# Optimization experiments

Measured on AMD Instinct MI355X. Metric: run time of the kernel, lower is better.

Reference implementation:

```python
import jax, jax.numpy as jnp
import numpy as np


def setup_inputs() -> dict:
    key = jax.random.key(0)
    k1, k2 = jax.random.split(key)
    _input = jax.random.normal(k1, (64, 8, 256, 256), dtype=jnp.float32)
    _filter = jax.random.normal(k2, (8, 8, 3, 3), dtype=jnp.float32)
    return {"_input": _input, "_filter": _filter}


def reference(_input, _filter):
    # The original module builds an im2col buffer with Python loops and does a
    # single GEMM; the math is exactly a stride-1, VALID-padding cross-correlation:
    #   out[n,m,i,j] = sum_{c,r,s} input[n,c,i+r,j+s] * filter[m,c,r,s]
    # Expressed as the efficient implicit-GEMM convolution primitive.
    out = jax.lax.conv_general_dilated(
        _input, _filter,
        window_strides=(1, 1),
        padding="VALID",
        dimension_numbers=("NCHW", "OIHW", "NCHW"),
    )
    return out  # (N, M, H-R+1, W-S+1)
```

## Files before the change

### kernel.cpp

```cpp
#include <hip/hip_runtime.h>


#define SLOT_HALFS (4 * 256 * 8)

typedef _Float16 half8 __attribute__((ext_vector_type(8)));
typedef float floatx4 __attribute__((ext_vector_type(4)));

__global__ __launch_bounds__(256, 3)
void conv2d_mfma_kernel(const float* __restrict__ inp,
                        const float* __restrict__ filt,
                        float* __restrict__ out) {
    __shared__ __align__(16) _Float16 s_in[3 * SLOT_HALFS + 64];

    const int tid    = threadIdx.x;
    const int ystrip = blockIdx.x * 32;
    const int n      = blockIdx.y;

    const float* in_n  = inp + (size_t)n * (8 * 256 * 256);
    float*       out_n = out + (size_t)n * (8 * 254 * 254);

    const int lane = tid & 63;
    const int w    = tid >> 6;
    const int lx   = lane & 15;
    const int g    = lane >> 4;

    half8 afrag[3];
    int roff[3], soff[3];
    #pragma unroll
    for (int kk = 0; kk < 3; ++kk) {
        int q  = kk * 4 + g;
        int qa = q > 8 ? 8 : q;
        roff[kk] = qa / 3;
        soff[kk] = qa - roff[kk] * 3;
        half8 a = {};
        if (q <= 8 && lx < 8) {
            #pragma unroll
            for (int j = 0; j < 8; ++j)
                a[j] = (_Float16)filt[lx * 72 + j * 9 + q];
        }
        afrag[kk] = a;
    }

    float v[4][8];
    auto load_chunk = [&](int ck) {
        #pragma unroll
        for (int k = 0; k < 4; ++k) {
            const int  iy = ystrip + ck * 4 + k;
            const bool ok = iy < 256;
            const float* p = in_n + iy * 256 + tid;
            #pragma unroll
            for (int c = 0; c < 8; ++c)
                v[k][c] = ok ? p[c * 65536] : 0.0f;
        }
    };
    auto write_chunk = [&](int ck) {
        _Float16* base = &s_in[(ck % 3) * SLOT_HALFS];
        #pragma unroll
        for (int k = 0; k < 4; ++k) {
            half8 h;
            #pragma unroll
            for (int c = 0; c < 8; ++c) h[c] = (_Float16)v[k][c];
            *reinterpret_cast<half8*>(&base[(k * 256 + tid) * 8]) = h;
        }
    };

    load_chunk(0); write_chunk(0);
    load_chunk(1); write_chunk(1);
    __syncthreads();

    for (int t = 0; t < 8; ++t) {
        if (t < 7) load_chunk(t + 2);

        const int ro = t * 4 + w;
        const int oy = ystrip + ro;

        const _Float16* bptr[3];
        #pragma unroll
        for (int kk = 0; kk < 3; ++kk) {
            int L    = ro + roff[kk];
            int slot = (L >> 2) % 3;
            bptr[kk] = &s_in[slot * SLOT_HALFS +
                             ((L & 3) * 256 + lx + soff[kk]) * 8];
        }

        const bool do_store = (g < 2) && (oy < 254);
        #pragma unroll
        for (int xg = 0; xg < 16; ++xg) {
            floatx4 acc = {0.0f, 0.0f, 0.0f, 0.0f};
            #pragma unroll
            for (int kk = 0; kk < 3; ++kk) {
                const half8 b =
                    *reinterpret_cast<const half8*>(bptr[kk] + xg * 128);
                acc = __builtin_amdgcn_mfma_f32_16x16x32_f16(
                          afrag[kk], b, acc, 0, 0, 0);
            }
            const int ox = xg * 16 + lx;
            if (do_store && ox < 254) {
                float* op = out_n + (g * 4) * 64516 + oy * 254 + ox;
                #pragma unroll
                for (int i = 0; i < 4; ++i)
                    op[i * 64516] = acc[i];
            }
        }

        if (t < 7) write_chunk(t + 2);
        __syncthreads();
    }
}

extern "C" void kernel_launch(void* const* d_in, const int* in_sizes, int n_in,
                              void* d_out, int out_size, void* d_ws, size_t ws_size,
                              hipStream_t stream) {
    const float* inp  = (const float*)d_in[0];
    const float* filt = (const float*)d_in[1];
    float* outp = (float*)d_out;

    dim3 grid(8, 64, 1);
    dim3 block(256);
    conv2d_mfma_kernel<<<grid, block, 0, stream>>>(inp, filt, outp);
}
```

Measured before the change: 306.8 us.

## Vectorize global loads, swizzle LDS layout, and stage output through shared memory

```diff
diff --git a/kernel.cpp b/kernel.cpp
--- a/kernel.cpp
+++ b/kernel.cpp
@@ -1,16 +1,17 @@
 #include <hip/hip_runtime.h>
 
-
-#define SLOT_HALFS (4 * 256 * 8)
 
 typedef _Float16 half8 __attribute__((ext_vector_type(8)));
 typedef float floatx4 __attribute__((ext_vector_type(4)));
 
-__global__ __launch_bounds__(256, 3)
+#define SLOT_H 8192
+
+__global__ __launch_bounds__(256, 2)
 void conv2d_mfma_kernel(const float* __restrict__ inp,
                         const float* __restrict__ filt,
                         float* __restrict__ out) {
-    __shared__ __align__(16) _Float16 s_in[3 * SLOT_HALFS + 64];
+    __shared__ __align__(16) _Float16 s_in[3 * SLOT_H];
+    __shared__ __align__(16) float    s_out[4 * 2048];
 
     const int tid    = threadIdx.x;
     const int ystrip = blockIdx.x * 32;
@@ -23,15 +24,24 @@
     const int w    = tid >> 6;
     const int lx   = lane & 15;
     const int g    = lane >> 4;
+    const int lx4  = tid & 63;
 
     half8 afrag[3];
-    int roff[3], soff[3];
+    int   roff[3];
+    int   loH[3][4];
     #pragma unroll
     for (int kk = 0; kk < 3; ++kk) {
         int q  = kk * 4 + g;
         int qa = q > 8 ? 8 : q;
         roff[kk] = qa / 3;
-        soff[kk] = qa - roff[kk] * 3;
+        int soff = qa - roff[kk] * 3;
+        int q0   = lx + soff;
+        int e    = (q0 & 3) ^ ((q0 >> 2) & 3);
+        int q0b  = q0 >> 4;
+        int baseH = (q0 >> 2) * 32;
+        #pragma unroll
+        for (int j = 0; j < 4; ++j)
+            loH[kk][j] = baseH + ((e ^ ((j + q0b) & 3)) << 3);
         half8 a = {};
         if (q <= 8 && lx < 8) {
             #pragma unroll
@@ -41,26 +51,28 @@
         afrag[kk] = a;
     }
 
-    float v[4][8];
+    float4 vv[8];
     auto load_chunk = [&](int ck) {
-        #pragma unroll
-        for (int k = 0; k < 4; ++k) {
-            const int  iy = ystrip + ck * 4 + k;
-            const bool ok = iy < 256;
-            const float* p = in_n + iy * 256 + tid;
+        const int iy = ystrip + ck * 4 + w;
+        if (iy < 256) {
+            const float* p = in_n + iy * 256 + lx4 * 4;
             #pragma unroll
             for (int c = 0; c < 8; ++c)
-                v[k][c] = ok ? p[c * 65536] : 0.0f;
+                vv[c] = *reinterpret_cast<const float4*>(p + c * 65536);
+        } else {
+            #pragma unroll
+            for (int c = 0; c < 8; ++c) vv[c] = make_float4(0.f,0.f,0.f,0.f);
         }
     };
     auto write_chunk = [&](int ck) {
-        _Float16* base = &s_in[(ck % 3) * SLOT_HALFS];
+        _Float16* base = &s_in[(ck % 3) * SLOT_H + w * 2048 + lx4 * 32];
+        const int sw = (lx4 & 3) ^ ((lx4 >> 2) & 3);
         #pragma unroll
-        for (int k = 0; k < 4; ++k) {
+        for (int i = 0; i < 4; ++i) {
             half8 h;
             #pragma unroll
-            for (int c = 0; c < 8; ++c) h[c] = (_Float16)v[k][c];
-            *reinterpret_cast<half8*>(&base[(k * 256 + tid) * 8]) = h;
+            for (int c = 0; c < 8; ++c) h[c] = (_Float16)vv[c][i];
+            *reinterpret_cast<half8*>(base + ((i ^ sw) << 3)) = h;
         }
     };
 
@@ -70,36 +82,47 @@
 
     for (int t = 0; t < 8; ++t) {
         if (t < 7) load_chunk(t + 2);
+        __builtin_amdgcn_sched_barrier(0);
 
         const int ro = t * 4 + w;
         const int oy = ystrip + ro;
 
-        const _Float16* bptr[3];
+        int ab[3][4];
         #pragma unroll
         for (int kk = 0; kk < 3; ++kk) {
             int L    = ro + roff[kk];
-            int slot = (L >> 2) % 3;
-            bptr[kk] = &s_in[slot * SLOT_HALFS +
-                             ((L & 3) * 256 + lx + soff[kk]) * 8];
+            int rbH  = ((L >> 2) % 3) * SLOT_H + (L & 3) * 2048;
+            #pragma unroll
+            for (int j = 0; j < 4; ++j) ab[kk][j] = rbH + loH[kk][j];
         }
 
-        const bool do_store = (g < 2) && (oy < 254);
+        const bool do_out = (g < 2) && (oy < 254);
         #pragma unroll
         for (int xg = 0; xg < 16; ++xg) {
-            floatx4 acc = {0.0f, 0.0f, 0.0f, 0.0f};
+            floatx4 acc = {0.f, 0.f, 0.f, 0.f};
             #pragma unroll
             for (int kk = 0; kk < 3; ++kk) {
-                const half8 b =
-                    *reinterpret_cast<const half8*>(bptr[kk] + xg * 128);
+                const half8 b = *reinterpret_cast<const half8*>(
+                    &s_in[ab[kk][xg & 3] + xg * 128]);
                 acc = __builtin_amdgcn_mfma_f32_16x16x32_f16(
                           afrag[kk], b, acc, 0, 0, 0);
             }
-            const int ox = xg * 16 + lx;
-            if (do_store && ox < 254) {
-                float* op = out_n + (g * 4) * 64516 + oy * 254 + ox;
+            if (do_out) {
                 #pragma unroll
                 for (int i = 0; i < 4; ++i)
-                    op[i * 64516] = acc[i];
+                    s_out[w * 2048 + (g * 4 + i) * 256 + xg * 16 + lx] = acc[i];
+            }
+        }
+
+        if (oy < 254) {
+            #pragma unroll
+            for (int m = 0; m < 8; ++m) {
+                float4 q4 = *reinterpret_cast<const float4*>(
+                    &s_out[w * 2048 + m * 256 + lane * 4]);
+                float* op = out_n + (size_t)m * 64516 + oy * 254 + lane * 4;
+                *reinterpret_cast<float2*>(op) = make_float2(q4.x, q4.y);
+                if (lane < 63)
+                    *reinterpret_cast<float2*>(op + 2) = make_float2(q4.z, q4.w);
             }
         }
 
```

Measured after the change: 258.3 us. 15.8% less time.
